# Optimization experiments

Hardware: AMD Instinct MI355X
Metric: run time of the kernel (lower is better)

## Reference

```python
import jax, jax.numpy as jnp
import numpy as np


def setup_inputs() -> dict:
    key = jax.random.key(0)
    k1, k2, k3, k4 = jax.random.split(key, 4)
    B, OUT, IN, K = 64, 4096, 25088, 32
    x = jax.random.normal(k1, (B, IN), dtype=jnp.float32)
    labels = jax.random.randint(k2, (OUT, IN), 0, K, dtype=jnp.int32)
    centroids = jax.random.normal(k3, (K,), dtype=jnp.float32)
    bias = jax.random.normal(k4, (OUT,), dtype=jnp.float32)
    return {"x": x, "labels": labels, "centroids": centroids, "bias": bias}


def reference(x, labels, centroids, bias):
    # Dequantize: reconstruct weight [OUT, IN] by looking labels up in the codebook
    W = centroids[labels]                      # [OUT, IN] gather
    # addmm(bias, x, W.T): [B, IN] @ [IN, OUT] + [OUT]
    return x @ W.T + bias
```

## Files before the change

kernel.cpp:

```cpp
#include <hip/hip_runtime.h>
#include <stdint.h>

typedef float f32x4 __attribute__((ext_vector_type(4)));
typedef short bf16x8 __attribute__((ext_vector_type(8)));
typedef int   i32x4  __attribute__((ext_vector_type(4)));

#define IN_DIM   25088
#define OUT_DIM  4096
#define BATCH    64
#define SPLITS   28
#define KBLK     64
#define NBLK     14
#define WG_N     128
#define LSTR     72

#define CONV_BLOCKS 784
#define PART_OFF   (4u << 20)

__device__ __forceinline__ uint32_t f2bf(float f) {
    uint32_t u = __builtin_bit_cast(uint32_t, f);
    return (u + 0x7FFFu + ((u >> 16) & 1u)) >> 16;
}

__global__ __launch_bounds__(256) void prep(const float* __restrict__ x,
                                            uint32_t* __restrict__ xb) {
    const size_t i = blockIdx.x * 256 + threadIdx.x;
    const float4 v0 = *(const float4*)(x + i * 8);
    const float4 v1 = *(const float4*)(x + i * 8 + 4);
    uint4 o;
    o.x = f2bf(v0.x) | (f2bf(v0.y) << 16);
    o.y = f2bf(v0.z) | (f2bf(v0.w) << 16);
    o.z = f2bf(v1.x) | (f2bf(v1.y) << 16);
    o.w = f2bf(v1.z) | (f2bf(v1.w) << 16);
    *(uint4*)(xb + i * 4) = o;
}

__global__ __launch_bounds__(256) void qlinear_main(
    const int*      __restrict__ labels,
    const float*    __restrict__ centroids,
    const uint16_t* __restrict__ xb,
    float*          __restrict__ partials)
{
    __shared__ __align__(16) uint32_t table[1024];
    __shared__ __align__(16) uint16_t wt[WG_N * LSTR];
    __shared__ __align__(16) uint16_t xt[BATCH * LSTR];

    const int t     = threadIdx.x;
    const int wgn   = blockIdx.x & 31;
    const int split = blockIdx.x >> 5;
    const int o0    = wgn * WG_N;
    const int kbase = split * (KBLK * NBLK);

    #pragma unroll
    for (int e = 0; e < 4; ++e) {
        const int i = t + 256 * e;
        table[i] = f2bf(centroids[i & 31]) | (f2bf(centroids[i >> 5]) << 16);
    }

    const int lane = t & 63;
    const int wave = t >> 6;
    const int ln   = lane & 15;
    const int lq   = lane >> 4;

    const int srow = t >> 3;
    const int skc  = (t & 7) * 8;

    const int xrow = t >> 2;
    const int xseg = (t & 3) * 16;

    const int* lbase[4];
    #pragma unroll
    for (int p = 0; p < 4; ++p)
        lbase[p] = labels + (size_t)(o0 + p * 32 + srow) * IN_DIM + kbase + skc;

    f32x4 acc[4][2] = {};

    i32x4 pl[4][2];
    #pragma unroll
    for (int p = 0; p < 4; ++p) {
        pl[p][0] = __builtin_nontemporal_load((const i32x4*)lbase[p]);
        pl[p][1] = __builtin_nontemporal_load((const i32x4*)lbase[p] + 1);
    }

    for (int blk = 0; blk < NBLK; ++blk) {
        const int k0 = kbase + blk * KBLK;

        i32x4 npl[4][2];
        if (blk + 1 < NBLK) {
            #pragma unroll
            for (int p = 0; p < 4; ++p) {
                const i32x4* lp = (const i32x4*)(lbase[p] + (blk + 1) * KBLK);
                npl[p][0] = __builtin_nontemporal_load(lp);
                npl[p][1] = __builtin_nontemporal_load(lp + 1);
            }
        }

        __syncthreads();

        #pragma unroll
        for (int p = 0; p < 4; ++p) {
            const int row = p * 32 + srow;
            uint4 w;
            w.x = table[(uint32_t)pl[p][0].x | ((uint32_t)pl[p][0].y << 5)];
            w.y = table[(uint32_t)pl[p][0].z | ((uint32_t)pl[p][0].w << 5)];
            w.z = table[(uint32_t)pl[p][1].x | ((uint32_t)pl[p][1].y << 5)];
            w.w = table[(uint32_t)pl[p][1].z | ((uint32_t)pl[p][1].w << 5)];
            *(uint4*)(wt + row * LSTR + skc) = w;
        }
        {
            const uint16_t* xp = xb + (size_t)xrow * IN_DIM + k0 + xseg;
            const bf16x8 v0 = *(const bf16x8*)xp;
            const bf16x8 v1 = *(const bf16x8*)(xp + 8);
            *(bf16x8*)(xt + xrow * LSTR + xseg)     = v0;
            *(bf16x8*)(xt + xrow * LSTR + xseg + 8) = v1;
        }
        __syncthreads();

        #pragma unroll
        for (int ks = 0; ks < 2; ++ks) {
            const int kk = ks * 32 + lq * 8;
            bf16x8 a[4], b[2];
            #pragma unroll
            for (int mt = 0; mt < 4; ++mt)
                a[mt] = *(const bf16x8*)(xt + (mt * 16 + ln) * LSTR + kk);
            #pragma unroll
            for (int nt = 0; nt < 2; ++nt)
                b[nt] = *(const bf16x8*)(wt + (wave * 32 + nt * 16 + ln) * LSTR + kk);
            #pragma unroll
            for (int mt = 0; mt < 4; ++mt)
                #pragma unroll
                for (int nt = 0; nt < 2; ++nt)
                    acc[mt][nt] = __builtin_amdgcn_mfma_f32_16x16x32_bf16(
                        a[mt], b[nt], acc[mt][nt], 0, 0, 0);
        }

        #pragma unroll
        for (int p = 0; p < 4; ++p) {
            pl[p][0] = npl[p][0];
            pl[p][1] = npl[p][1];
        }
    }

    float* pout = partials + (size_t)split * BATCH * OUT_DIM;
    #pragma unroll
    for (int mt = 0; mt < 4; ++mt)
        #pragma unroll
        for (int nt = 0; nt < 2; ++nt) {
            const int o = o0 + wave * 32 + nt * 16 + ln;
            #pragma unroll
            for (int r = 0; r < 4; ++r)
                __builtin_nontemporal_store(
                    acc[mt][nt][r],
                    pout + (size_t)(mt * 16 + lq * 4 + r) * OUT_DIM + o);
        }
}

__global__ __launch_bounds__(256) void reduce_out(
    const float* __restrict__ partials,
    const float* __restrict__ bias,
    float*       __restrict__ out) {
    const int g  = blockIdx.x * 256 + threadIdx.x;
    const int o4 = g & (OUT_DIM / 4 - 1);
    f32x4 s = *((const f32x4*)bias + o4);
    const f32x4* p = (const f32x4*)partials + g;
    #pragma unroll
    for (int sp = 0; sp < SPLITS; ++sp)
        s += p[(size_t)sp * (BATCH * OUT_DIM / 4)];
    *((f32x4*)out + g) = s;
}

extern "C" void kernel_launch(void* const* d_in, const int* in_sizes, int n_in,
                              void* d_out, int out_size, void* d_ws, size_t ws_size,
                              hipStream_t stream) {
    const float* x         = (const float*)d_in[0];
    const int*   labels    = (const int*)d_in[1];
    const float* centroids = (const float*)d_in[2];
    const float* bias      = (const float*)d_in[3];
    float* out = (float*)d_out;

    uint32_t* xb       = (uint32_t*)d_ws;
    float*    partials = (float*)((char*)d_ws + PART_OFF);

    prep<<<CONV_BLOCKS, 256, 0, stream>>>(x, xb);
    qlinear_main<<<32 * SPLITS, 256, 0, stream>>>(labels, centroids,
                                                  (const uint16_t*)xb, partials);
    reduce_out<<<BATCH * OUT_DIM / 4 / 256, 256, 0, stream>>>(partials, bias, out);
}
```

Before: 553.4 us.

## Use larger K blocks, fewer splits, and load x fragments directly from global

Raises the K block from 64 to 256 and halves the split count from 28 to 14, so each workgroup covers 1792 K elements over 7 blocks and fewer partials must be reduced. The label loads are reorganised so each wave reads 8 rows with lanes contiguous along K. The x tile is no longer staged in shared memory; its MFMA fragments are read straight from global memory with a two-step register prefetch. This cuts LDS traffic and barriers and halves the partials written and reduced, but the grid shrinks to 448 workgroups, the LDS tile grows, and label prefetch overlaps less with compute.

```diff
diff --git a/kernel.cpp b/kernel.cpp
--- a/kernel.cpp
+++ b/kernel.cpp
@@ -8,11 +8,12 @@
 #define IN_DIM   25088
 #define OUT_DIM  4096
 #define BATCH    64
-#define SPLITS   28
-#define KBLK     64
-#define NBLK     14
+#define SPLITS   14
+#define CHUNK    1792
+#define KBLK     256
+#define NBLK     7
 #define WG_N     128
-#define LSTR     72
+#define LSTR     264
 
 #define CONV_BLOCKS 784
 #define PART_OFF   (4u << 20)
@@ -43,13 +44,12 @@
 {
     __shared__ __align__(16) uint32_t table[1024];
     __shared__ __align__(16) uint16_t wt[WG_N * LSTR];
-    __shared__ __align__(16) uint16_t xt[BATCH * LSTR];
 
     const int t     = threadIdx.x;
     const int wgn   = blockIdx.x & 31;
     const int split = blockIdx.x >> 5;
     const int o0    = wgn * WG_N;
-    const int kbase = split * (KBLK * NBLK);
+    const int kbase = split * CHUNK;
 
     #pragma unroll
     for (int e = 0; e < 4; ++e) {
@@ -62,82 +62,84 @@
     const int ln   = lane & 15;
     const int lq   = lane >> 4;
 
-    const int srow = t >> 3;
-    const int skc  = (t & 7) * 8;
+    const int rbase = wave * 8;
+    const int* lb = labels + (size_t)(o0 + rbase) * IN_DIM + kbase + lane * 4;
 
-    const int xrow = t >> 2;
-    const int xseg = (t & 3) * 16;
-
-    const int* lbase[4];
+    const uint16_t* xp[4];
     #pragma unroll
-    for (int p = 0; p < 4; ++p)
-        lbase[p] = labels + (size_t)(o0 + p * 32 + srow) * IN_DIM + kbase + skc;
+    for (int mt = 0; mt < 4; ++mt)
+        xp[mt] = xb + (size_t)(mt * 16 + ln) * IN_DIM + kbase + lq * 8;
 
     f32x4 acc[4][2] = {};
 
-    i32x4 pl[4][2];
+    i32x4 cur[8];
     #pragma unroll
-    for (int p = 0; p < 4; ++p) {
-        pl[p][0] = __builtin_nontemporal_load((const i32x4*)lbase[p]);
-        pl[p][1] = __builtin_nontemporal_load((const i32x4*)lbase[p] + 1);
-    }
+    for (int j = 0; j < 8; ++j)
+        cur[j] = __builtin_nontemporal_load((const i32x4*)(lb + (size_t)j * IN_DIM));
 
     for (int blk = 0; blk < NBLK; ++blk) {
-        const int k0 = kbase + blk * KBLK;
-
-        i32x4 npl[4][2];
-        if (blk + 1 < NBLK) {
-            #pragma unroll
-            for (int p = 0; p < 4; ++p) {
-                const i32x4* lp = (const i32x4*)(lbase[p] + (blk + 1) * KBLK);
-                npl[p][0] = __builtin_nontemporal_load(lp);
-                npl[p][1] = __builtin_nontemporal_load(lp + 1);
-            }
-        }
-
         __syncthreads();
 
+        const int* lblk = lb + blk * KBLK;
         #pragma unroll
-        for (int p = 0; p < 4; ++p) {
-            const int row = p * 32 + srow;
-            uint4 w;
-            w.x = table[(uint32_t)pl[p][0].x | ((uint32_t)pl[p][0].y << 5)];
-            w.y = table[(uint32_t)pl[p][0].z | ((uint32_t)pl[p][0].w << 5)];
-            w.z = table[(uint32_t)pl[p][1].x | ((uint32_t)pl[p][1].y << 5)];
-            w.w = table[(uint32_t)pl[p][1].z | ((uint32_t)pl[p][1].w << 5)];
-            *(uint4*)(wt + row * LSTR + skc) = w;
-        }
-        {
-            const uint16_t* xp = xb + (size_t)xrow * IN_DIM + k0 + xseg;
-            const bf16x8 v0 = *(const bf16x8*)xp;
-            const bf16x8 v1 = *(const bf16x8*)(xp + 8);
-            *(bf16x8*)(xt + xrow * LSTR + xseg)     = v0;
-            *(bf16x8*)(xt + xrow * LSTR + xseg + 8) = v1;
+        for (int s = 0; s < 4; ++s) {
+            i32x4 nxt[8];
+            if (s < 3) {
+                const int* lp = lblk + (size_t)(s + 1) * 32 * IN_DIM;
+                #pragma unroll
+                for (int j = 0; j < 8; ++j)
+                    nxt[j] = __builtin_nontemporal_load((const i32x4*)(lp + (size_t)j * IN_DIM));
+            }
+            #pragma unroll
+            for (int j = 0; j < 8; ++j) {
+                const int row = s * 32 + rbase + j;
+                uint2 w;
+                w.x = table[(uint32_t)cur[j].x | ((uint32_t)cur[j].y << 5)];
+                w.y = table[(uint32_t)cur[j].z | ((uint32_t)cur[j].w << 5)];
+                *(uint2*)(wt + row * LSTR + lane * 4) = w;
+            }
+            if (s < 3) {
+                #pragma unroll
+                for (int j = 0; j < 8; ++j) cur[j] = nxt[j];
+            }
         }
         __syncthreads();
 
+        if (blk + 1 < NBLK) {
+            const int* lp = lb + (size_t)(blk + 1) * KBLK;
+            #pragma unroll
+            for (int j = 0; j < 8; ++j)
+                cur[j] = __builtin_nontemporal_load((const i32x4*)(lp + (size_t)j * IN_DIM));
+        }
+
+        const size_t xoff = (size_t)blk * KBLK;
+        bf16x8 a0[4], a1[4];
         #pragma unroll
-        for (int ks = 0; ks < 2; ++ks) {
-            const int kk = ks * 32 + lq * 8;
-            bf16x8 a[4], b[2];
-            #pragma unroll
-            for (int mt = 0; mt < 4; ++mt)
-                a[mt] = *(const bf16x8*)(xt + (mt * 16 + ln) * LSTR + kk);
+        for (int mt = 0; mt < 4; ++mt) {
+            a0[mt] = *(const bf16x8*)(xp[mt] + xoff);
+            a1[mt] = *(const bf16x8*)(xp[mt] + xoff + 32);
+        }
+        #pragma unroll
+        for (int ks = 0; ks < 8; ++ks) {
+            bf16x8 a2[4];
+            if (ks + 2 < 8) {
+                #pragma unroll
+                for (int mt = 0; mt < 4; ++mt)
+                    a2[mt] = *(const bf16x8*)(xp[mt] + xoff + (ks + 2) * 32);
+            }
+            bf16x8 b[2];
             #pragma unroll
             for (int nt = 0; nt < 2; ++nt)
-                b[nt] = *(const bf16x8*)(wt + (wave * 32 + nt * 16 + ln) * LSTR + kk);
+                b[nt] = *(const bf16x8*)(wt + (wave * 32 + nt * 16 + ln) * LSTR
+                                            + ks * 32 + lq * 8);
             #pragma unroll
             for (int mt = 0; mt < 4; ++mt)
                 #pragma unroll
                 for (int nt = 0; nt < 2; ++nt)
                     acc[mt][nt] = __builtin_amdgcn_mfma_f32_16x16x32_bf16(
-                        a[mt], b[nt], acc[mt][nt], 0, 0, 0);
-        }
-
-        #pragma unroll
-        for (int p = 0; p < 4; ++p) {
-            pl[p][0] = npl[p][0];
-            pl[p][1] = npl[p][1];
+                        a0[mt], b[nt], acc[mt][nt], 0, 0, 0);
+            #pragma unroll
+            for (int mt = 0; mt < 4; ++mt) { a0[mt] = a1[mt]; a1[mt] = a2[mt]; }
         }
     }
 
```

Result: no change. 555.0 us (+0.3%).

## Pre-pack labels into 16-bit pair codes and read x operands directly from global

Applied to the files above, without the earlier changes.

Adds a repack kernel that compresses each pair of int32 labels into a 16-bit table index, so the main GEMM kernel streams a quarter of the label bytes. The main kernel doubles its K block, drops the LDS staging of x, and loads x fragments straight from global memory. The repack runs on every call and reads the full label tensor plus writes a packed copy, so total memory traffic rises unless the main kernel's savings outweigh that extra pass.

```diff
diff --git a/kernel.cpp b/kernel.cpp
--- a/kernel.cpp
+++ b/kernel.cpp
@@ -8,18 +8,36 @@
 #define IN_DIM   25088
 #define OUT_DIM  4096
 #define BATCH    64
+#define PAIRS    (IN_DIM / 2)
 #define SPLITS   28
-#define KBLK     64
-#define NBLK     14
+#define CHUNK    896
+#define KBLK     128
+#define NBLK     7
 #define WG_N     128
-#define LSTR     72
+#define LSTR     136
 
 #define CONV_BLOCKS 784
-#define PART_OFF   (4u << 20)
+#define RPK_BLOCKS  25088
+#define PK_OFF     (4u << 20)
+#define PART_OFF   (112u << 20)
 
 __device__ __forceinline__ uint32_t f2bf(float f) {
     uint32_t u = __builtin_bit_cast(uint32_t, f);
     return (u + 0x7FFFu + ((u >> 16) & 1u)) >> 16;
+}
+
+__global__ __launch_bounds__(256) void repack(const int* __restrict__ labels,
+                                              uint32_t* __restrict__ pk) {
+    const size_t base = (size_t)blockIdx.x * 4096;
+    const int t = threadIdx.x;
+    #pragma unroll
+    for (int j = 0; j < 4; ++j) {
+        const i32x4 v = __builtin_nontemporal_load(
+            (const i32x4*)(labels + base) + j * 256 + t);
+        const uint32_t p = (uint32_t)(v.x | (v.y << 5))
+                         | ((uint32_t)(v.z | (v.w << 5)) << 16);
+        __builtin_nontemporal_store(p, pk + base / 4 + j * 256 + t);
+    }
 }
 
 __global__ __launch_bounds__(256) void prep(const float* __restrict__ x,
@@ -36,20 +54,18 @@
 }
 
 __global__ __launch_bounds__(256) void qlinear_main(
-    const int*      __restrict__ labels,
+    const uint16_t* __restrict__ pk,
     const float*    __restrict__ centroids,
     const uint16_t* __restrict__ xb,
     float*          __restrict__ partials)
 {
     __shared__ __align__(16) uint32_t table[1024];
     __shared__ __align__(16) uint16_t wt[WG_N * LSTR];
-    __shared__ __align__(16) uint16_t xt[BATCH * LSTR];
 
     const int t     = threadIdx.x;
     const int wgn   = blockIdx.x & 31;
     const int split = blockIdx.x >> 5;
     const int o0    = wgn * WG_N;
-    const int kbase = split * (KBLK * NBLK);
 
     #pragma unroll
     for (int e = 0; e < 4; ++e) {
@@ -63,36 +79,33 @@
     const int lq   = lane >> 4;
 
     const int srow = t >> 3;
-    const int skc  = (t & 7) * 8;
+    const int seg  = t & 7;
 
-    const int xrow = t >> 2;
-    const int xseg = (t & 3) * 16;
-
-    const int* lbase[4];
+    const uint16_t* lbase[4];
     #pragma unroll
     for (int p = 0; p < 4; ++p)
-        lbase[p] = labels + (size_t)(o0 + p * 32 + srow) * IN_DIM + kbase + skc;
+        lbase[p] = pk + (size_t)(o0 + p * 32 + srow) * PAIRS
+                      + split * (CHUNK / 2) + seg * 8;
+
+    const uint16_t* xp[4];
+    #pragma unroll
+    for (int mt = 0; mt < 4; ++mt)
+        xp[mt] = xb + (size_t)(mt * 16 + ln) * IN_DIM + split * CHUNK + lq * 8;
 
     f32x4 acc[4][2] = {};
 
-    i32x4 pl[4][2];
+    i32x4 pl[4];
     #pragma unroll
-    for (int p = 0; p < 4; ++p) {
-        pl[p][0] = __builtin_nontemporal_load((const i32x4*)lbase[p]);
-        pl[p][1] = __builtin_nontemporal_load((const i32x4*)lbase[p] + 1);
-    }
+    for (int p = 0; p < 4; ++p)
+        pl[p] = __builtin_nontemporal_load((const i32x4*)lbase[p]);
 
     for (int blk = 0; blk < NBLK; ++blk) {
-        const int k0 = kbase + blk * KBLK;
-
-        i32x4 npl[4][2];
+        i32x4 npl[4];
         if (blk + 1 < NBLK) {
             #pragma unroll
-            for (int p = 0; p < 4; ++p) {
-                const i32x4* lp = (const i32x4*)(lbase[p] + (blk + 1) * KBLK);
-                npl[p][0] = __builtin_nontemporal_load(lp);
-                npl[p][1] = __builtin_nontemporal_load(lp + 1);
-            }
+            for (int p = 0; p < 4; ++p)
+                npl[p] = __builtin_nontemporal_load(
+                    (const i32x4*)(lbase[p] + (blk + 1) * (KBLK / 2)));
         }
 
         __syncthreads();
@@ -100,29 +113,27 @@
         #pragma unroll
         for (int p = 0; p < 4; ++p) {
             const int row = p * 32 + srow;
-            uint4 w;
-            w.x = table[(uint32_t)pl[p][0].x | ((uint32_t)pl[p][0].y << 5)];
-            w.y = table[(uint32_t)pl[p][0].z | ((uint32_t)pl[p][0].w << 5)];
-            w.z = table[(uint32_t)pl[p][1].x | ((uint32_t)pl[p][1].y << 5)];
-            w.w = table[(uint32_t)pl[p][1].z | ((uint32_t)pl[p][1].w << 5)];
-            *(uint4*)(wt + row * LSTR + skc) = w;
-        }
-        {
-            const uint16_t* xp = xb + (size_t)xrow * IN_DIM + k0 + xseg;
-            const bf16x8 v0 = *(const bf16x8*)xp;
-            const bf16x8 v1 = *(const bf16x8*)(xp + 8);
-            *(bf16x8*)(xt + xrow * LSTR + xseg)     = v0;
-            *(bf16x8*)(xt + xrow * LSTR + xseg + 8) = v1;
+            const uint32_t u0 = (uint32_t)pl[p].x, u1 = (uint32_t)pl[p].y;
+            const uint32_t u2 = (uint32_t)pl[p].z, u3 = (uint32_t)pl[p].w;
+            uint4 w0, w1;
+            w0.x = table[u0 & 0xFFFF]; w0.y = table[u0 >> 16];
+            w0.z = table[u1 & 0xFFFF]; w0.w = table[u1 >> 16];
+            w1.x = table[u2 & 0xFFFF]; w1.y = table[u2 >> 16];
+            w1.z = table[u3 & 0xFFFF]; w1.w = table[u3 >> 16];
+            uint16_t* dst = wt + row * LSTR + seg * 16;
+            *(uint4*)dst       = w0;
+            *(uint4*)(dst + 8) = w1;
         }
         __syncthreads();
 
+        const int xoff = blk * KBLK;
         #pragma unroll
-        for (int ks = 0; ks < 2; ++ks) {
+        for (int ks = 0; ks < 4; ++ks) {
             const int kk = ks * 32 + lq * 8;
             bf16x8 a[4], b[2];
             #pragma unroll
             for (int mt = 0; mt < 4; ++mt)
-                a[mt] = *(const bf16x8*)(xt + (mt * 16 + ln) * LSTR + kk);
+                a[mt] = *(const bf16x8*)(xp[mt] + xoff + ks * 32);
             #pragma unroll
             for (int nt = 0; nt < 2; ++nt)
                 b[nt] = *(const bf16x8*)(wt + (wave * 32 + nt * 16 + ln) * LSTR + kk);
@@ -135,10 +146,7 @@
         }
 
         #pragma unroll
-        for (int p = 0; p < 4; ++p) {
-            pl[p][0] = npl[p][0];
-            pl[p][1] = npl[p][1];
-        }
+        for (int p = 0; p < 4; ++p) pl[p] = npl[p];
     }
 
     float* pout = partials + (size_t)split * BATCH * OUT_DIM;
@@ -179,10 +187,12 @@
     float* out = (float*)d_out;
 
     uint32_t* xb       = (uint32_t*)d_ws;
+    uint32_t* pkw      = (uint32_t*)((char*)d_ws + PK_OFF);
     float*    partials = (float*)((char*)d_ws + PART_OFF);
 
+    repack<<<RPK_BLOCKS, 256, 0, stream>>>(labels, pkw);
     prep<<<CONV_BLOCKS, 256, 0, stream>>>(x, xb);
-    qlinear_main<<<32 * SPLITS, 256, 0, stream>>>(labels, centroids,
+    qlinear_main<<<32 * SPLITS, 256, 0, stream>>>((const uint16_t*)pkw, centroids,
                                                   (const uint16_t*)xb, partials);
     reduce_out<<<BATCH * OUT_DIM / 4 / 256, 256, 0, stream>>>(partials, bias, out);
 }
```

Measured after the change: 601.8 us. +8.8%, slower.
